# Performance work log

Measured on AMD Instinct MI355X. Metric: run time of the kernel, lower is better.

## Reference

```python
import jax, jax.numpy as jnp
import numpy as np

B, S, D, H = 4, 1024, 1024, 16
E = 8                 # num_experts
FF1 = 4096            # d_hidden * expansion_factor * 2 (swiglu in)
FF2 = 2048            # d_hidden * expansion_factor (swiglu out / linear2 in)
TEMP = 0.5            # gating temperature
RMS_EPS_GATE = float(np.finfo(np.float32).eps)  # torch RMSNorm default eps
NORM_EPS = 1e-8       # layer_norm_eps


def setup_inputs() -> dict:
    key = jax.random.key(0)
    ks = jax.random.split(key, 8)
    s = 0.02
    return {
        "x": jax.random.normal(ks[0], (B, S, D), jnp.float32),
        "w_qkv": jax.random.normal(ks[1], (3 * D, D), jnp.float32) * s,
        "w_out": jax.random.normal(ks[2], (D, D), jnp.float32) * s,
        "norm1_w": jnp.ones((D,), jnp.float32),
        "norm2_w": jnp.ones((D,), jnp.float32),
        "gate_w": jax.random.normal(ks[3], (E, D), jnp.float32) * s,
        "gate_b": jnp.zeros((E,), jnp.float32),
        "gate_rms_w": jnp.ones((E,), jnp.float32),
        "w1": jax.random.normal(ks[4], (E, D, FF1), jnp.float32) * s,
        "w2": jax.random.normal(ks[5], (E, FF2, D), jnp.float32) * s,
    }


def _rmsnorm(x, w, eps):
    return x * w * jax.lax.rsqrt(jnp.mean(x * x, axis=-1, keepdims=True) + eps)


def _attn(h, w_qkv, w_out):
    qkv = h @ w_qkv.T                              # [B,S,3D]
    q, k, v = jnp.split(qkv, 3, axis=-1)
    dh = D // H
    q = q.reshape(B, S, H, dh)
    k = k.reshape(B, S, H, dh)
    v = v.reshape(B, S, H, dh)
    scores = jnp.einsum("bqhd,bkhd->bhqk", q, k) / jnp.sqrt(jnp.float32(dh))
    p = jax.nn.softmax(scores, axis=-1)
    o = jnp.einsum("bhqk,bkhd->bqhd", p, v).reshape(B, S, D)
    return o @ w_out.T


def _moe(h, gate_w, gate_b, gate_rms_w, w1, w2):
    xf = h.reshape(-1, D)                          # [N,D]
    logits = _rmsnorm(xf @ gate_w.T + gate_b, gate_rms_w, RMS_EPS_GATE)
    gates = jax.nn.softmax(logits / TEMP, axis=-1)  # [N,E]
    top_g, _ = jax.lax.top_k(gates, 1)              # top_k = 1
    # capacity dispatch mask degenerates to all-ones (capacity >= 1), so
    # normalized gate = g / (g + 1e-6)
    g = top_g[:, 0] / (top_g[:, 0] + 1e-6)          # [N]
    h1 = jnp.einsum("nd,edf->nef", xf, w1)          # [N,E,FF1]
    a, b = jnp.split(h1, 2, axis=-1)                # SwiGLU
    act = a * jax.nn.silu(b)                        # [N,E,FF2]
    outs = jnp.einsum("nef,efd->ned", act, w2)      # [N,E,D]
    # gate broadcasts over the expert axis (as in the original code)
    comb = outs.sum(axis=1) * g[:, None]
    return comb.reshape(h.shape)


def reference(x, w_qkv, w_out, norm1_w, norm2_w, gate_w, gate_b, gate_rms_w, w1, w2):
    # pre-norm transformer block, eval mode (no dropout / gating noise)
    x = x + _attn(_rmsnorm(x, norm1_w, NORM_EPS), w_qkv, w_out)
    x = x + _moe(_rmsnorm(x, norm2_w, NORM_EPS), gate_w, gate_b, gate_rms_w, w1, w2)
    return x
```

## Files before the change

kernel.cpp:

```cpp
#include <hip/hip_runtime.h>
#include <hip/hip_bf16.h>
#include <math.h>

typedef __bf16 bf16_t;
typedef __bf16 bf16x8 __attribute__((ext_vector_type(8)));
typedef float f32x4 __attribute__((ext_vector_type(4)));

typedef const __attribute__((address_space(1))) void* gptr_t;
typedef __attribute__((address_space(3))) void* lptr_t;

#define MFMA16(a, b, c) __builtin_amdgcn_mfma_f32_16x16x32_bf16((a), (b), (c), 0, 0, 0)
#define BAR() __builtin_amdgcn_s_barrier()
#define WAIT_LGKM()                                        \
  do {                                                     \
    asm volatile("s_waitcnt lgkmcnt(0)" ::: "memory");     \
    __builtin_amdgcn_sched_barrier(0);                     \
  } while (0)
#define WAIT_VM4()                                         \
  do {                                                     \
    asm volatile("s_waitcnt vmcnt(4)" ::: "memory");       \
    __builtin_amdgcn_sched_barrier(0);                     \
  } while (0)
#define WAIT_VM8()                                         \
  do {                                                     \
    asm volatile("s_waitcnt vmcnt(8)" ::: "memory");       \
    __builtin_amdgcn_sched_barrier(0);                     \
  } while (0)
#define WAIT_VM0()                                         \
  do {                                                     \
    asm volatile("s_waitcnt vmcnt(0)" ::: "memory");       \
    __builtin_amdgcn_sched_barrier(0);                     \
  } while (0)

__device__ __forceinline__ void gload_lds16(const bf16_t* g, bf16_t* l) {
  __builtin_amdgcn_global_load_lds((gptr_t)g, (lptr_t)l, 16, 0, 0);
}

__global__ __launch_bounds__(256) void conv_kernel(const float* __restrict__ in,
                                                   bf16_t* __restrict__ out, int n4) {
  int i = blockIdx.x * 256 + threadIdx.x;
  if (i >= n4) return;
  float4 v = ((const float4*)in)[i];
  bf16_t* o = out + (size_t)i * 4;
  o[0] = (bf16_t)v.x; o[1] = (bf16_t)v.y; o[2] = (bf16_t)v.z; o[3] = (bf16_t)v.w;
}

__global__ __launch_bounds__(256) void transp_w1(const float* __restrict__ in,
                                                 bf16_t* __restrict__ out) {
  __shared__ float tile[32][33];
  const float* ip = in + (size_t)blockIdx.z * 1024 * 4096;
  bf16_t* op = out + (size_t)blockIdx.z * 4096 * 1024;
  int tx = threadIdx.x, ty = threadIdx.y;
  int r0 = blockIdx.y * 32, c0 = blockIdx.x * 32;
#pragma unroll
  for (int i = 0; i < 32; i += 8)
    tile[ty + i][tx] = ip[(size_t)(r0 + ty + i) * 4096 + c0 + tx];
  __syncthreads();
#pragma unroll
  for (int i = 0; i < 32; i += 8) {
    int c = c0 + ty + i;
    int p = (c < 2048) ? ((c >> 5) * 64 + (c & 31))
                       : (((c - 2048) >> 5) * 64 + 32 + ((c - 2048) & 31));
    op[(size_t)p * 1024 + r0 + tx] = (bf16_t)tile[tx][ty + i];
  }
}

__global__ __launch_bounds__(256) void transp_w2(const float* __restrict__ in,
                                                 bf16_t* __restrict__ out) {
  __shared__ float tile[32][33];
  const float* ip = in + (size_t)blockIdx.z * 2048 * 1024;
  int tx = threadIdx.x, ty = threadIdx.y;
  int r0 = blockIdx.y * 32, c0 = blockIdx.x * 32;
#pragma unroll
  for (int i = 0; i < 32; i += 8)
    tile[ty + i][tx] = ip[(size_t)(r0 + ty + i) * 1024 + c0 + tx];
  __syncthreads();
#pragma unroll
  for (int i = 0; i < 32; i += 8)
    out[(size_t)(c0 + ty + i) * 16384 + blockIdx.z * 2048 + r0 + tx] = (bf16_t)tile[tx][ty + i];
}

__global__ __launch_bounds__(256) void rmsnorm_kernel(const float* __restrict__ x,
                                                      const float* __restrict__ w,
                                                      bf16_t* __restrict__ out, float eps) {
  int row = blockIdx.x;
  int t = threadIdx.x;
  const float4* xr = (const float4*)(x + (size_t)row * 1024);
  float4 v = xr[t];
  float ss = v.x * v.x + v.y * v.y + v.z * v.z + v.w * v.w;
#pragma unroll
  for (int off = 1; off < 64; off <<= 1) ss += __shfl_xor(ss, off, 64);
  __shared__ float red[4];
  int wave = t >> 6, lane = t & 63;
  if (lane == 0) red[wave] = ss;
  __syncthreads();
  ss = red[0] + red[1] + red[2] + red[3];
  float inv = rsqrtf(ss * (1.0f / 1024.0f) + eps);
  float4 wv = ((const float4*)w)[t];
  bf16_t* o = out + (size_t)row * 1024 + t * 4;
  o[0] = (bf16_t)(v.x * wv.x * inv);
  o[1] = (bf16_t)(v.y * wv.y * inv);
  o[2] = (bf16_t)(v.z * wv.z * inv);
  o[3] = (bf16_t)(v.w * wv.w * inv);
}

template <int EPI>
__global__ __launch_bounds__(512, 2) void gemm256(const bf16_t* __restrict__ A,
                                                  const bf16_t* __restrict__ Bt,
                                                  void* __restrict__ C,
                                                  const float* __restrict__ resid,
                                                  int M, int N, int K, int lda, int ldb) {
  __shared__ bf16_t As[2][256 * 64];
  __shared__ bf16_t Bs[2][256 * 64];
  const int tid = threadIdx.x;
  const int wave = tid >> 6, lane = tid & 63;

  const int gx = gridDim.x, gy = gridDim.y;
  int nwg = gx * gy * gridDim.z;
  int lin = blockIdx.x + gx * (blockIdx.y + gy * blockIdx.z);
  int wid = ((nwg & 7) == 0) ? ((lin & 7) * (nwg >> 3) + (lin >> 3)) : lin;
  const int bx = wid % gx;
  const int by = (wid / gx) % gy;
  const int bz = wid / (gx * gy);

  const int m0 = by * 256, n0 = bx * 256;
  const int wr = (wave >> 2) * 128, wc = (wave & 3) * 64;
  const int fr = lane & 15, fq = lane >> 4;

  if (EPI == 4) Bt += (size_t)bz * 4096 * 1024;
  if (EPI == 5) {
    A += (size_t)bz * K;
    Bt += (size_t)bz * K;
  }

  const int srw = lane >> 3;
  const int sgc = (lane & 7) ^ srw;
  const bf16_t* aBase = A + (size_t)(m0 + wave * 8 + srw) * lda + sgc * 8;
  const bf16_t* bBase = Bt + (size_t)(n0 + wave * 8 + srw) * ldb + sgc * 8;

  auto stageA = [&](bf16_t* buf, int kt) {
#pragma unroll
    for (int i = 0; i < 4; ++i) {
      int r = i * 64;
      gload_lds16(aBase + (size_t)r * lda + kt * 64, &buf[(r + wave * 8) * 64]);
    }
  };
  auto stageB = [&](bf16_t* buf, int kt) {
#pragma unroll
    for (int i = 0; i < 4; ++i) {
      int r = i * 64;
      gload_lds16(bBase + (size_t)r * ldb + kt * 64, &buf[(r + wave * 8) * 64]);
    }
  };

  f32x4 acc[8][4] = {};
  bf16x8 a_[4][2], b_[4][2];

  auto readA = [&](int b, int mh) {
#pragma unroll
    for (int q = 0; q < 4; ++q)
#pragma unroll
      for (int ks = 0; ks < 2; ++ks) {
        int r = wr + mh * 64 + q * 16 + fr;
        a_[q][ks] = *(const bf16x8*)&As[b][r * 64 + (((fq + ks * 4) ^ (fr & 7)) << 3)];
      }
  };
  auto readB = [&](int b, int nh) {
#pragma unroll
    for (int q = 0; q < 2; ++q)
#pragma unroll
      for (int ks = 0; ks < 2; ++ks) {
        int r = wc + nh * 32 + q * 16 + fr;
        b_[nh * 2 + q][ks] = *(const bf16x8*)&Bs[b][r * 64 + (((fq + ks * 4) ^ (fr & 7)) << 3)];
      }
  };
  auto mfma16x = [&](int mh, int nh) {
    __builtin_amdgcn_s_setprio(1);
#pragma unroll
    for (int q = 0; q < 4; ++q)
#pragma unroll
      for (int n = 0; n < 2; ++n)
#pragma unroll
        for (int ks = 0; ks < 2; ++ks)
          acc[mh * 4 + q][nh * 2 + n] =
              MFMA16(a_[q][ks], b_[nh * 2 + n][ks], acc[mh * 4 + q][nh * 2 + n]);
    __builtin_amdgcn_s_setprio(0);
  };

  const int NKT = K >> 6;
  stageB(Bs[0], 0);
  stageA(As[0], 0);
  stageB(Bs[1], 1);
  stageA(As[1], 1);
  WAIT_VM8();
  BAR();
  readA(0, 0);
  readB(0, 0);

  for (int it = 0; it < (NKT >> 1) - 1; ++it) {
    const int t2 = 2 * it + 2, t3 = 2 * it + 3;
    WAIT_LGKM(); mfma16x(0, 0); readB(0, 1); BAR();
    WAIT_LGKM(); mfma16x(0, 1); readA(0, 1); BAR();
    WAIT_LGKM(); mfma16x(1, 0); stageB(Bs[0], t2); WAIT_VM4(); BAR();
    WAIT_LGKM(); mfma16x(1, 1); readA(1, 0); readB(1, 0); stageA(As[0], t2); BAR();
    WAIT_LGKM(); mfma16x(0, 0); readB(1, 1); BAR();
    WAIT_LGKM(); mfma16x(0, 1); readA(1, 1); BAR();
    WAIT_LGKM(); mfma16x(1, 0); stageB(Bs[1], t3); WAIT_VM4(); BAR();
    WAIT_LGKM(); mfma16x(1, 1); readA(0, 0); readB(0, 0); stageA(As[1], t3); BAR();
  }

  WAIT_LGKM(); mfma16x(0, 0); readB(0, 1); BAR();
  WAIT_LGKM(); mfma16x(0, 1); readA(0, 1); BAR();
  WAIT_LGKM(); mfma16x(1, 0); WAIT_VM0(); BAR();
  WAIT_LGKM(); mfma16x(1, 1); readA(1, 0); readB(1, 0); BAR();
  WAIT_LGKM(); mfma16x(0, 0); readB(1, 1); BAR();
  WAIT_LGKM(); mfma16x(0, 1); readA(1, 1); BAR();
  WAIT_LGKM(); mfma16x(1, 0); BAR();
  WAIT_LGKM(); mfma16x(1, 1);

  if (EPI == 4) {
    bf16_t* act = (bf16_t*)C;
    int strip = (n0 >> 6) + (wave & 3);
#pragma unroll
    for (int mq = 0; mq < 8; ++mq)
#pragma unroll
      for (int n = 0; n < 2; ++n)
#pragma unroll
        for (int j = 0; j < 4; ++j) {
          size_t row = (size_t)(m0 + wr + mq * 16 + fq * 4 + j);
          size_t col = (size_t)bz * 2048 + strip * 32 + n * 16 + fr;
          float a = acc[mq][n][j], b = acc[mq][n + 2][j];
          act[row * 16384 + col] = (bf16_t)(a * (b / (1.0f + __expf(-b))));
        }
    return;
  }
#pragma unroll
  for (int mq = 0; mq < 8; ++mq)
#pragma unroll
    for (int n = 0; n < 4; ++n)
#pragma unroll
      for (int j = 0; j < 4; ++j) {
        size_t row = (size_t)(m0 + wr + mq * 16 + fq * 4 + j);
        size_t col = (size_t)(n0 + wc + n * 16 + fr);
        float v = acc[mq][n][j];
        if (EPI == 0)
          ((bf16_t*)C)[row * N + col] = (bf16_t)v;
        else if (EPI == 1)
          ((float*)C)[row * N + col] = resid[row * N + col] + v;
        else if (EPI == 5)
          ((float*)C + (size_t)bz * M * N)[row * N + col] = v;
      }
}

__global__ __launch_bounds__(256) void attn_kernel(const bf16_t* __restrict__ qkv,
                                                   bf16_t* __restrict__ o) {
  const int S = 1024, LD = 3072;
  int qt = blockIdx.x, bh = blockIdx.y;
  int b = bh >> 4, h = bh & 15;
  int tid = threadIdx.x, wave = tid >> 6, lane = tid & 63;
  int fr = lane & 15, fq = lane >> 4, kg = fq * 8;
  int q0 = qt * 64 + wave * 16;
  const bf16_t* qb = qkv + (size_t)b * S * LD + h * 64;
  const bf16_t* kb = qb + 1024;
  const bf16_t* vb = qb + 2048;

  __shared__ bf16_t Ks[64 * 64];
  __shared__ bf16_t Vt[64 * 64];
  __shared__ bf16_t Ps[4][16 * 72];

  bf16x8 qf0 = *(const bf16x8*)&qb[(size_t)(q0 + fr) * LD + kg];
  bf16x8 qf1 = *(const bf16x8*)&qb[(size_t)(q0 + fr) * LD + 32 + kg];

  f32x4 acc[4] = {};
  float mrow[4] = {-1e30f, -1e30f, -1e30f, -1e30f};
  float ssum[4] = {0.f, 0.f, 0.f, 0.f};

  for (int k0 = 0; k0 < S; k0 += 64) {
#pragma unroll
    for (int cc = 0; cc < 2; ++cc) {
      int c = tid + cc * 256;
      int r = c >> 3, ch = c & 7;
      *(bf16x8*)&Ks[r * 64 + ((ch ^ (r & 7)) << 3)] =
          *(const bf16x8*)&kb[(size_t)(k0 + r) * LD + ch * 8];
      bf16x8 vv = *(const bf16x8*)&vb[(size_t)(k0 + r) * LD + ch * 8];
#pragma unroll
      for (int i = 0; i < 8; ++i) {
        int d = ch * 8 + i;
        int cs = ((r >> 3) ^ (d >> 3) ^ (d & 7)) & 7;
        Vt[d * 64 + cs * 8 + (r & 7)] = vv[i];
      }
    }
    __syncthreads();

    f32x4 s[4];
#pragma unroll
    for (int kc = 0; kc < 4; ++kc) {
      int row = kc * 16 + fr, sw = row & 7;
      bf16x8 kf0 = *(const bf16x8*)&Ks[row * 64 + ((fq ^ sw) << 3)];
      bf16x8 kf1 = *(const bf16x8*)&Ks[row * 64 + (((4 + fq) ^ sw) << 3)];
      f32x4 z = {};
      z = MFMA16(qf0, kf0, z);
      z = MFMA16(qf1, kf1, z);
      s[kc] = z * 0.125f;
    }
    float pmax[4], psum[4], scl[4];
#pragma unroll
    for (int j = 0; j < 4; ++j)
      pmax[j] = fmaxf(fmaxf(s[0][j], s[1][j]), fmaxf(s[2][j], s[3][j]));
#pragma unroll
    for (int off = 1; off < 16; off <<= 1)
#pragma unroll
      for (int j = 0; j < 4; ++j) pmax[j] = fmaxf(pmax[j], __shfl_xor(pmax[j], off, 64));
#pragma unroll
    for (int j = 0; j < 4; ++j) {
      float nm = fmaxf(mrow[j], pmax[j]);
      scl[j] = __expf(mrow[j] - nm);
      mrow[j] = nm;
      psum[j] = 0.f;
    }
#pragma unroll
    for (int kc = 0; kc < 4; ++kc)
#pragma unroll
      for (int j = 0; j < 4; ++j) {
        float p = __expf(s[kc][j] - mrow[j]);
        psum[j] += p;
        Ps[wave][(fq * 4 + j) * 72 + kc * 16 + fr] = (bf16_t)p;
      }
#pragma unroll
    for (int off = 1; off < 16; off <<= 1)
#pragma unroll
      for (int j = 0; j < 4; ++j) psum[j] += __shfl_xor(psum[j], off, 64);
#pragma unroll
    for (int j = 0; j < 4; ++j) ssum[j] = ssum[j] * scl[j] + psum[j];
#pragma unroll
    for (int n = 0; n < 4; ++n)
#pragma unroll
      for (int j = 0; j < 4; ++j) acc[n][j] *= scl[j];
    asm volatile("s_waitcnt lgkmcnt(0)" ::: "memory");
    bf16x8 pa[2];
#pragma unroll
    for (int ks = 0; ks < 2; ++ks) pa[ks] = *(const bf16x8*)&Ps[wave][fr * 72 + ks * 32 + kg];
#pragma unroll
    for (int n = 0; n < 4; ++n) {
      int d = n * 16 + fr;
      int swd = ((d >> 3) ^ (d & 7)) & 7;
#pragma unroll
      for (int ks = 0; ks < 2; ++ks) {
        bf16x8 vbf = *(const bf16x8*)&Vt[d * 64 + (((ks * 4 + fq) ^ swd) << 3)];
        acc[n] = MFMA16(pa[ks], vbf, acc[n]);
      }
    }
    __syncthreads();
  }
#pragma unroll
  for (int n = 0; n < 4; ++n)
#pragma unroll
    for (int j = 0; j < 4; ++j) {
      size_t row = (size_t)b * S + q0 + fq * 4 + j;
      o[row * 1024 + h * 64 + n * 16 + fr] = (bf16_t)(acc[n][j] / ssum[j]);
    }
}

__global__ __launch_bounds__(256) void gate_kernel(const bf16_t* __restrict__ hn,
                                                   const float* __restrict__ gw,
                                                   const float* __restrict__ gb,
                                                   const float* __restrict__ grms,
                                                   float* __restrict__ g) {
  int n = blockIdx.x * 4 + (threadIdx.x >> 6);
  int lane = threadIdx.x & 63;
  const bf16_t* xr = hn + (size_t)n * 1024;
  float acc[8] = {};
  for (int i = lane; i < 1024; i += 64) {
    float xv = (float)xr[i];
#pragma unroll
    for (int e = 0; e < 8; ++e) acc[e] += xv * gw[e * 1024 + i];
  }
#pragma unroll
  for (int e = 0; e < 8; ++e)
    for (int off = 1; off < 64; off <<= 1) acc[e] += __shfl_xor(acc[e], off, 64);
  float l[8], ms = 0.f;
#pragma unroll
  for (int e = 0; e < 8; ++e) {
    l[e] = acc[e] + gb[e];
    ms += l[e] * l[e];
  }
  float inv = rsqrtf(ms * 0.125f + 1.1920928955078125e-07f);
  float mx = -1e30f;
#pragma unroll
  for (int e = 0; e < 8; ++e) {
    l[e] = l[e] * inv * grms[e] * 2.0f;
    mx = fmaxf(mx, l[e]);
  }
  float s = 0.f;
#pragma unroll
  for (int e = 0; e < 8; ++e) s += __expf(l[e] - mx);
  float t = 1.0f / s;
  if (lane == 0) g[n] = t / (t + 1e-6f);
}

__global__ __launch_bounds__(256) void combine4(const float* __restrict__ moep,
                                                const float* __restrict__ x1,
                                                const float* __restrict__ g,
                                                float* __restrict__ out, int Mc) {
  size_t i4 = (size_t)blockIdx.x * 256 + threadIdx.x;
  size_t row = i4 >> 8;
  size_t stride4 = (size_t)Mc * 256;
  float4 s = {0.f, 0.f, 0.f, 0.f};
#pragma unroll
  for (int z = 0; z < 4; ++z) {
    float4 v = ((const float4*)moep)[z * stride4 + i4];
    s.x += v.x; s.y += v.y; s.z += v.z; s.w += v.w;
  }
  float gv = g[row];
  float4 xv = ((const float4*)x1)[i4];
  float4 r;
  r.x = xv.x + s.x * gv;
  r.y = xv.y + s.y * gv;
  r.z = xv.z + s.z * gv;
  r.w = xv.w + s.w * gv;
  ((float4*)out)[i4] = r;
}

extern "C" void kernel_launch(void* const* d_in, const int* in_sizes, int n_in,
                              void* d_out, int out_size, void* d_ws, size_t ws_size,
                              hipStream_t stream) {
  const float* x = (const float*)d_in[0];
  const float* w_qkv = (const float*)d_in[1];
  const float* w_out = (const float*)d_in[2];
  const float* norm1_w = (const float*)d_in[3];
  const float* norm2_w = (const float*)d_in[4];
  const float* gate_w = (const float*)d_in[5];
  const float* gate_b = (const float*)d_in[6];
  const float* gate_rms = (const float*)d_in[7];
  const float* w1 = (const float*)d_in[8];
  const float* w2 = (const float*)d_in[9];
  float* out = (float*)d_out;

  const size_t baseB = (8ull * 4096 * 1024 + 1024ull * 16384 + 3072ull * 1024 +
                        1024ull * 1024 + 4096ull * 1024) * 2 +
                       4096ull * 1024 * 4 + 4096 * 4;
  int cc = 4;
  if (ws_size >= baseB + 4096ull * 16384 * 2 + 4ull * 4096 * 1024 * 4)
    cc = 1;
  else if (ws_size >= baseB + 2048ull * 16384 * 2 + 4ull * 2048 * 1024 * 4)
    cc = 2;
  const int Mc = 4096 / cc;

  char* ws = (char*)d_ws;
  size_t off = 0;
  auto alloc = [&](size_t bytes) {
    char* p = ws + off;
    off += bytes;
    return p;
  };
  bf16_t* w1t = (bf16_t*)alloc(8ull * 4096 * 1024 * 2);
  bf16_t* w2t = (bf16_t*)alloc(1024ull * 16384 * 2);
  bf16_t* wqkvb = (bf16_t*)alloc(3072ull * 1024 * 2);
  bf16_t* woutb = (bf16_t*)alloc(1024ull * 1024 * 2);
  bf16_t* hn = (bf16_t*)alloc(4096ull * 1024 * 2);
  float* x1 = (float*)alloc(4096ull * 1024 * 4);
  float* gbuf = (float*)alloc(4096ull * 4);
  bf16_t* act = (bf16_t*)alloc((size_t)Mc * 16384 * 2);
  float* moep = (float*)alloc(4ull * Mc * 1024 * 4);
  bf16_t* qkvb = (bf16_t*)act;
  bf16_t* attno = (bf16_t*)moep;

  conv_kernel<<<3072, 256, 0, stream>>>(w_qkv, wqkvb, 3072 * 1024 / 4);
  conv_kernel<<<1024, 256, 0, stream>>>(w_out, woutb, 1024 * 1024 / 4);
  transp_w1<<<dim3(128, 32, 8), dim3(32, 8), 0, stream>>>(w1, w1t);
  transp_w2<<<dim3(32, 64, 8), dim3(32, 8), 0, stream>>>(w2, w2t);

  rmsnorm_kernel<<<4096, 256, 0, stream>>>(x, norm1_w, hn, 1e-8f);
  gemm256<0><<<dim3(12, 16), 512, 0, stream>>>(hn, wqkvb, qkvb, nullptr, 4096, 3072, 1024,
                                               1024, 1024);
  attn_kernel<<<dim3(16, 64), 256, 0, stream>>>(qkvb, attno);
  gemm256<1><<<dim3(4, 16), 512, 0, stream>>>(attno, woutb, x1, x, 4096, 1024, 1024, 1024,
                                              1024);

  rmsnorm_kernel<<<4096, 256, 0, stream>>>(x1, norm2_w, hn, 1e-8f);
  gate_kernel<<<1024, 256, 0, stream>>>(hn, gate_w, gate_b, gate_rms, gbuf);
  for (int c = 0; c < cc; ++c) {
    gemm256<4><<<dim3(16, Mc / 256, 8), 512, 0, stream>>>(
        hn + (size_t)c * Mc * 1024, w1t, act, nullptr, Mc, 4096, 1024, 1024, 1024);
    gemm256<5><<<dim3(4, Mc / 256, 4), 512, 0, stream>>>(
        act, w2t, moep, nullptr, Mc, 1024, 4096, 16384, 16384);
    combine4<<<Mc, 256, 0, stream>>>(moep, x1 + (size_t)c * Mc * 1024, gbuf + (size_t)c * Mc,
                                     out + (size_t)c * Mc * 1024, Mc);
  }
}
```

Before: 604.9 us.

## Widen weight transposes, tile-swizzle expert GEMM grid, enlarge attention blocks

```diff
diff --git a/kernel.cpp b/kernel.cpp
--- a/kernel.cpp
+++ b/kernel.cpp
@@ -47,37 +47,58 @@
 
 __global__ __launch_bounds__(256) void transp_w1(const float* __restrict__ in,
                                                  bf16_t* __restrict__ out) {
-  __shared__ float tile[32][33];
+  __shared__ float tile[64][65];
   const float* ip = in + (size_t)blockIdx.z * 1024 * 4096;
   bf16_t* op = out + (size_t)blockIdx.z * 4096 * 1024;
-  int tx = threadIdx.x, ty = threadIdx.y;
-  int r0 = blockIdx.y * 32, c0 = blockIdx.x * 32;
-#pragma unroll
-  for (int i = 0; i < 32; i += 8)
-    tile[ty + i][tx] = ip[(size_t)(r0 + ty + i) * 4096 + c0 + tx];
+  int t = threadIdx.x;
+  int r0 = blockIdx.y * 64, c0 = blockIdx.x * 64;
+  int lr = t >> 4, lc4 = (t & 15) * 4;
+#pragma unroll
+  for (int p = 0; p < 4; ++p) {
+    float4 v = *(const float4*)&ip[(size_t)(r0 + p * 16 + lr) * 4096 + c0 + lc4];
+    tile[p * 16 + lr][lc4 + 0] = v.x;
+    tile[p * 16 + lr][lc4 + 1] = v.y;
+    tile[p * 16 + lr][lc4 + 2] = v.z;
+    tile[p * 16 + lr][lc4 + 3] = v.w;
+  }
   __syncthreads();
-#pragma unroll
-  for (int i = 0; i < 32; i += 8) {
-    int c = c0 + ty + i;
-    int p = (c < 2048) ? ((c >> 5) * 64 + (c & 31))
-                       : (((c - 2048) >> 5) * 64 + 32 + ((c - 2048) & 31));
-    op[(size_t)p * 1024 + r0 + tx] = (bf16_t)tile[tx][ty + i];
+  int c = t >> 2, rs = (t & 3) * 16;
+  int cg = c0 + c;
+  int pc = (cg < 2048) ? ((cg >> 5) * 64 + (cg & 31))
+                       : (((cg - 2048) >> 5) * 64 + 32 + ((cg - 2048) & 31));
+#pragma unroll
+  for (int h = 0; h < 2; ++h) {
+    bf16x8 v;
+#pragma unroll
+    for (int i = 0; i < 8; ++i) v[i] = (bf16_t)tile[rs + h * 8 + i][c];
+    *(bf16x8*)&op[(size_t)pc * 1024 + r0 + rs + h * 8] = v;
   }
 }
 
 __global__ __launch_bounds__(256) void transp_w2(const float* __restrict__ in,
                                                  bf16_t* __restrict__ out) {
-  __shared__ float tile[32][33];
+  __shared__ float tile[64][65];
   const float* ip = in + (size_t)blockIdx.z * 2048 * 1024;
-  int tx = threadIdx.x, ty = threadIdx.y;
-  int r0 = blockIdx.y * 32, c0 = blockIdx.x * 32;
-#pragma unroll
-  for (int i = 0; i < 32; i += 8)
-    tile[ty + i][tx] = ip[(size_t)(r0 + ty + i) * 1024 + c0 + tx];
+  int t = threadIdx.x;
+  int r0 = blockIdx.y * 64, c0 = blockIdx.x * 64;
+  int lr = t >> 4, lc4 = (t & 15) * 4;
+#pragma unroll
+  for (int p = 0; p < 4; ++p) {
+    float4 v = *(const float4*)&ip[(size_t)(r0 + p * 16 + lr) * 1024 + c0 + lc4];
+    tile[p * 16 + lr][lc4 + 0] = v.x;
+    tile[p * 16 + lr][lc4 + 1] = v.y;
+    tile[p * 16 + lr][lc4 + 2] = v.z;
+    tile[p * 16 + lr][lc4 + 3] = v.w;
+  }
   __syncthreads();
-#pragma unroll
-  for (int i = 0; i < 32; i += 8)
-    out[(size_t)(c0 + ty + i) * 16384 + blockIdx.z * 2048 + r0 + tx] = (bf16_t)tile[tx][ty + i];
+  int c = t >> 2, rs = (t & 3) * 16;
+#pragma unroll
+  for (int h = 0; h < 2; ++h) {
+    bf16x8 v;
+#pragma unroll
+    for (int i = 0; i < 8; ++i) v[i] = (bf16_t)tile[rs + h * 8 + i][c];
+    *(bf16x8*)&out[(size_t)(c0 + c) * 16384 + blockIdx.z * 2048 + r0 + rs + h * 8] = v;
+  }
 }
 
 __global__ __launch_bounds__(256) void rmsnorm_kernel(const float* __restrict__ x,
@@ -119,9 +140,18 @@
   int nwg = gx * gy * gridDim.z;
   int lin = blockIdx.x + gx * (blockIdx.y + gy * blockIdx.z);
   int wid = ((nwg & 7) == 0) ? ((lin & 7) * (nwg >> 3) + (lin >> 3)) : lin;
-  const int bx = wid % gx;
-  const int by = (wid / gx) % gy;
-  const int bz = wid / (gx * gy);
+  int bx, by, bz;
+  if (EPI == 4 && gx == 16 && gy == 16 && gridDim.z == 8) {
+    int local = wid & 255;
+    int st = local >> 4, wi = local & 15;
+    bx = (st & 3) * 4 + (wi & 3);
+    by = (st >> 2) * 4 + (wi >> 2);
+    bz = wid >> 8;
+  } else {
+    bx = wid % gx;
+    by = (wid / gx) % gy;
+    bz = wid / (gx * gy);
+  }
 
   const int m0 = by * 256, n0 = bx * 256;
   const int wr = (wave >> 2) * 128, wc = (wave & 3) * 64;
@@ -252,21 +282,21 @@
       }
 }
 
-__global__ __launch_bounds__(256) void attn_kernel(const bf16_t* __restrict__ qkv,
+__global__ __launch_bounds__(512) void attn_kernel(const bf16_t* __restrict__ qkv,
                                                    bf16_t* __restrict__ o) {
   const int S = 1024, LD = 3072;
   int qt = blockIdx.x, bh = blockIdx.y;
   int b = bh >> 4, h = bh & 15;
   int tid = threadIdx.x, wave = tid >> 6, lane = tid & 63;
   int fr = lane & 15, fq = lane >> 4, kg = fq * 8;
-  int q0 = qt * 64 + wave * 16;
+  int q0 = qt * 128 + wave * 16;
   const bf16_t* qb = qkv + (size_t)b * S * LD + h * 64;
   const bf16_t* kb = qb + 1024;
   const bf16_t* vb = qb + 2048;
 
   __shared__ bf16_t Ks[64 * 64];
   __shared__ bf16_t Vt[64 * 64];
-  __shared__ bf16_t Ps[4][16 * 72];
+  __shared__ bf16_t Ps[8][16 * 72];
 
   bf16x8 qf0 = *(const bf16x8*)&qb[(size_t)(q0 + fr) * LD + kg];
   bf16x8 qf1 = *(const bf16x8*)&qb[(size_t)(q0 + fr) * LD + 32 + kg];
@@ -276,9 +306,8 @@
   float ssum[4] = {0.f, 0.f, 0.f, 0.f};
 
   for (int k0 = 0; k0 < S; k0 += 64) {
-#pragma unroll
-    for (int cc = 0; cc < 2; ++cc) {
-      int c = tid + cc * 256;
+    {
+      int c = tid;
       int r = c >> 3, ch = c & 7;
       *(bf16x8*)&Ks[r * 64 + ((ch ^ (r & 7)) << 3)] =
           *(const bf16x8*)&kb[(size_t)(k0 + r) * LD + ch * 8];
@@ -467,13 +496,13 @@
 
   conv_kernel<<<3072, 256, 0, stream>>>(w_qkv, wqkvb, 3072 * 1024 / 4);
   conv_kernel<<<1024, 256, 0, stream>>>(w_out, woutb, 1024 * 1024 / 4);
-  transp_w1<<<dim3(128, 32, 8), dim3(32, 8), 0, stream>>>(w1, w1t);
-  transp_w2<<<dim3(32, 64, 8), dim3(32, 8), 0, stream>>>(w2, w2t);
+  transp_w1<<<dim3(64, 16, 8), 256, 0, stream>>>(w1, w1t);
+  transp_w2<<<dim3(16, 32, 8), 256, 0, stream>>>(w2, w2t);
 
   rmsnorm_kernel<<<4096, 256, 0, stream>>>(x, norm1_w, hn, 1e-8f);
   gemm256<0><<<dim3(12, 16), 512, 0, stream>>>(hn, wqkvb, qkvb, nullptr, 4096, 3072, 1024,
                                                1024, 1024);
-  attn_kernel<<<dim3(16, 64), 256, 0, stream>>>(qkvb, attno);
+  attn_kernel<<<dim3(8, 64), 512, 0, stream>>>(qkvb, attno);
   gemm256<1><<<dim3(4, 16), 512, 0, stream>>>(attno, woutb, x1, x, 4096, 1024, 1024, 1024,
                                               1024);
 
```

Result: no change. 601.3 us (-0.6%).
